# Performance work log

Hardware: AMD Instinct MI355X
Metric: run time of the kernel (lower is better)

Reference implementation:

```python
import jax, jax.numpy as jnp
import numpy as np
from jax import lax

HID = 1024
EXP = 2
INTER = HID * EXP          # 2048
STATE = 64
DT_RANK = INTER            # must equal INTER for the dt_bias broadcast in source
EPS = 1e-5


def _lin_w(k, i, o):
    return jax.random.normal(k, (i, o), jnp.float32) * (1.0 / np.sqrt(i))


def setup_inputs() -> dict:
    key = jax.random.key(0)
    ks = jax.random.split(key, 16)
    B, L = 4, 4096
    return {
        "x": jax.random.normal(ks[0], (B, L, HID), jnp.float32),
        "condition": jax.random.normal(ks[1], (B, HID), jnp.float32),
        "ln_g": jnp.ones((HID,), jnp.float32),
        "ln_b": jnp.zeros((HID,), jnp.float32),
        "W_in": _lin_w(ks[2], HID, 2 * INTER),
        "b_in": jnp.zeros((2 * INTER,), jnp.float32),
        "conv_w": jax.random.normal(ks[3], (INTER, 1, 3), jnp.float32) * 0.3,  # depthwise OIW
        "conv_b": jnp.zeros((INTER,), jnp.float32),
        "W_dt": _lin_w(ks[4], INTER, DT_RANK),
        "b_dt": jnp.zeros((DT_RANK,), jnp.float32),
        "dt_bias": jax.random.uniform(ks[5], (INTER,), jnp.float32),
        "A_log": jnp.log(jnp.arange(1, STATE + 1, dtype=jnp.float32)),
        "Dp": jnp.ones((INTER,), jnp.float32),
        "W_B": _lin_w(ks[6], INTER, STATE),
        "b_B": jnp.zeros((STATE,), jnp.float32),
        "W_C": _lin_w(ks[7], INTER, STATE),
        "b_C": jnp.zeros((STATE,), jnp.float32),
        "W_cond": _lin_w(ks[8], HID, INTER),
        "b_cond": jnp.zeros((INTER,), jnp.float32),
        "W_out": _lin_w(ks[9], INTER, HID),
        "b_out": jnp.zeros((HID,), jnp.float32),
    }


def _selective_scan(xp, W_dt, b_dt, dt_bias, A_log, Dp, W_B, b_B, W_C, b_C):
    B, L, Dm = xp.shape
    dt = jax.nn.softplus(xp @ W_dt + b_dt + dt_bias)          # [B,L,INTER]
    dt = jnp.mean(dt, axis=-1, keepdims=True)                  # [B,L,1]
    A = -jnp.exp(A_log)                                        # [STATE]
    A_disc = jnp.exp(A * dt)                                   # [B,L,STATE]
    Bx = (xp @ W_B + b_B) * dt * jnp.mean(xp, axis=-1, keepdims=True)  # B_disc * x_mean
    C = xp @ W_C + b_C                                         # [B,L,STATE]

    def step(h, inp):
        a, b, c = inp                                          # each [B,STATE]
        h = a * h + b
        return h, jnp.sum(c * h, axis=-1)                      # y_t: [B]

    h0 = jnp.zeros((B, STATE), xp.dtype)
    _, ys = lax.scan(step, h0, (A_disc.transpose(1, 0, 2),
                                Bx.transpose(1, 0, 2),
                                C.transpose(1, 0, 2)))         # ys: [L,B]
    y = ys.T[..., None]                                        # [B,L,1]
    return y + xp * Dp                                         # broadcast to [B,L,INTER]


def reference(x, condition, ln_g, ln_b, W_in, b_in, conv_w, conv_b, W_dt, b_dt,
              dt_bias, A_log, Dp, W_B, b_B, W_C, b_C, W_cond, b_cond, W_out, b_out):
    residual = x
    mu = jnp.mean(x, axis=-1, keepdims=True)
    var = jnp.mean((x - mu) ** 2, axis=-1, keepdims=True)
    xn = (x - mu) / jnp.sqrt(var + EPS) * ln_g + ln_b

    xproj2 = xn @ W_in + b_in                                  # [B,L,2*INTER]
    xproj, gate = jnp.split(xproj2, 2, axis=-1)

    # depthwise conv1d, kernel 3, padding 1
    xc = xproj.transpose(0, 2, 1)                              # [B,INTER,L]
    xc = lax.conv_general_dilated(xc, conv_w, (1,), [(1, 1)],
                                  dimension_numbers=("NCH", "OIH", "NCH"),
                                  feature_group_count=INTER)
    xc = xc + conv_b[None, :, None]
    xproj = xc.transpose(0, 2, 1)

    xproj = jax.nn.silu(xproj)
    xproj = xproj + (condition @ W_cond + b_cond)[:, None, :]

    y = _selective_scan(xproj, W_dt, b_dt, dt_bias, A_log, Dp, W_B, b_B, W_C, b_C)
    y = y * jax.nn.silu(gate)
    y = y @ W_out + b_out                                      # dropout is identity in eval
    return residual + y
```

## Files before the change

### kernel.cpp

```cpp
#include <hip/hip_runtime.h>
#include <stdint.h>

#define HID   1024
#define INTER 2048
#define NQK   4096
#define STATE 64
#define BSZ   4
#define LEN   4096
#define RTOT  (BSZ*LEN)
#define NCAT  2176
#define LC    128
#define NCH   (LEN/LC)

typedef unsigned short u16;
typedef u16   u16x4 __attribute__((ext_vector_type(4)));
typedef u16   u16x8 __attribute__((ext_vector_type(8)));
typedef float f32x4 __attribute__((ext_vector_type(4)));

__device__ __forceinline__ u16 f2bf(float f) {
  uint32_t u = __float_as_uint(f);
  u += 0x7fffu + ((u >> 16) & 1u);
  return (u16)(u >> 16);
}
__device__ __forceinline__ float bf2f(u16 h) {
  return __uint_as_float(((uint32_t)h) << 16);
}

typedef __attribute__((address_space(1))) void gvoid;
typedef __attribute__((address_space(3))) void lvoid;
__device__ __forceinline__ void gload16(const void* g, void* l) {
  __builtin_amdgcn_global_load_lds((gvoid*)(uintptr_t)g, (lvoid*)l, 16, 0, 0);
}

__device__ __forceinline__ void mfma16(f32x4 a, f32x4 b, f32x4& c) {
  asm volatile("v_mfma_f32_16x16x32_bf16 %0, %1, %2, %0" : "+v"(c) : "v"(a), "v"(b));
}

__global__ __launch_bounds__(256) void wconvT_kernel(const float* __restrict__ src,
                                                     u16* __restrict__ dst, int K, int N) {
  __shared__ float t[32][33];
  int tx = threadIdx.x & 31, ty = threadIdx.x >> 5;
  int n0 = blockIdx.x * 32, k0 = blockIdx.y * 32;
#pragma unroll
  for (int i = 0; i < 4; ++i)
    t[ty + 8*i][tx] = src[(size_t)(k0 + ty + 8*i) * N + n0 + tx];
  __syncthreads();
#pragma unroll
  for (int i = 0; i < 4; ++i)
    dst[(size_t)(n0 + ty + 8*i) * K + k0 + tx] = f2bf(t[tx][ty + 8*i]);
}

__global__ void bcat_kernel(const float* b_dt, const float* dt_bias, const float* b_B,
                            const float* b_C, float* bcat) {
  int i = blockIdx.x * 256 + threadIdx.x;
  if (i >= NCAT) return;
  float v;
  if (i < INTER) v = b_dt[i] + dt_bias[i];
  else if (i < INTER + STATE) v = b_B[i - INTER];
  else v = b_C[i - INTER - STATE];
  bcat[i] = v;
}

__global__ __launch_bounds__(256) void cond_kernel(const float* __restrict__ condition,
    const float* __restrict__ W, const float* __restrict__ bias, float* __restrict__ out) {
  int b = blockIdx.y;
  int j = blockIdx.x * 256 + threadIdx.x;
  float acc = bias[j];
  const float* crow = condition + b * HID;
  for (int k = 0; k < HID; ++k)
    acc = fmaf(crow[k], W[(size_t)k * INTER + j], acc);
  out[b * INTER + j] = acc;
}

__global__ __launch_bounds__(256) void ln_kernel(const float* __restrict__ x,
    const float* __restrict__ g, const float* __restrict__ bb, u16* __restrict__ xn) {
  int r = blockIdx.x;
  int tid = threadIdx.x;
  const float4 v = ((const float4*)(x + (size_t)r * HID))[tid];
  float s = v.x + v.y + v.z + v.w;
  float sq = v.x*v.x + v.y*v.y + v.z*v.z + v.w*v.w;
  for (int o = 32; o; o >>= 1) { s += __shfl_xor(s, o); sq += __shfl_xor(sq, o); }
  __shared__ float ps[4], pq[4];
  int wid = tid >> 6, lane = tid & 63;
  if (lane == 0) { ps[wid] = s; pq[wid] = sq; }
  __syncthreads();
  s = ps[0] + ps[1] + ps[2] + ps[3];
  sq = pq[0] + pq[1] + pq[2] + pq[3];
  float mu = s * (1.f / HID);
  float var = sq * (1.f / HID) - mu * mu;
  float rstd = rsqrtf(var + 1e-5f);
  int c = tid * 4;
  u16x4 ov;
  ov.x = f2bf((v.x - mu) * rstd * g[c+0] + bb[c+0]);
  ov.y = f2bf((v.y - mu) * rstd * g[c+1] + bb[c+1]);
  ov.z = f2bf((v.z - mu) * rstd * g[c+2] + bb[c+2]);
  ov.w = f2bf((v.w - mu) * rstd * g[c+3] + bb[c+3]);
  *(u16x4*)(xn + (size_t)r * HID + c) = ov;
}

template<int EPI>
__global__ __launch_bounds__(256) void gemm_bt(
    const u16* __restrict__ A, const u16* __restrict__ Bt, int K,
    const float* __restrict__ bias,
    u16* __restrict__ out0, u16* __restrict__ out1,
    float* __restrict__ dtsum, float* __restrict__ Bmat, float* __restrict__ Cmat,
    const float* __restrict__ resid, float* __restrict__ outf)
{
  __shared__ u16 lA[128 * 32];
  __shared__ u16 lB[128 * 32];
  const int tid = threadIdx.x;
  const int lane = tid & 63;
  const int wid = tid >> 6;
  const int wm = wid >> 1, wn = wid & 1;
  const int lr = lane & 15, lk = lane >> 4;
  const int col0 = blockIdx.x * 128;
  const int row0 = blockIdx.y * 128;
  const int wbase = tid & 192;

  f32x4 acc[4][4];
#pragma unroll
  for (int i = 0; i < 4; ++i)
#pragma unroll
    for (int j = 0; j < 4; ++j) acc[i][j] = (f32x4){0.f, 0.f, 0.f, 0.f};

  const size_t arow = (size_t)row0 * K;
  const size_t brow = (size_t)col0 * K;

  asm volatile("s_nop 7");
  for (int kt = 0; kt < K; kt += 32) {
    __syncthreads();
#pragma unroll
    for (int j = 0; j < 2; ++j) {
      int cbase = j * 256 + wbase;
      int chunk = cbase + lane;
      gload16(A + arow + (size_t)(chunk >> 2) * K + kt + (chunk & 3) * 8, &lA[cbase * 8]);
    }
#pragma unroll
    for (int j = 0; j < 2; ++j) {
      int cbase = j * 256 + wbase;
      int chunk = cbase + lane;
      gload16(Bt + brow + (size_t)(chunk >> 2) * K + kt + (chunk & 3) * 8, &lB[cbase * 8]);
    }
    __syncthreads();
    f32x4 aF[4], bF[4];
#pragma unroll
    for (int f = 0; f < 4; ++f)
      aF[f] = *(const f32x4*)&lA[(wm * 64 + f * 16 + lr) * 32 + lk * 8];
#pragma unroll
    for (int f = 0; f < 4; ++f)
      bF[f] = *(const f32x4*)&lB[(wn * 64 + f * 16 + lr) * 32 + lk * 8];
#pragma unroll
    for (int fm = 0; fm < 4; ++fm)
#pragma unroll
      for (int fn = 0; fn < 4; ++fn)
        mfma16(aF[fm], bF[fn], acc[fm][fn]);
  }
  asm volatile("s_nop 7\n\ts_nop 7\n\ts_nop 7");

  const int rb = row0 + wm * 64;
  const int cb = col0 + wn * 64;

  if constexpr (EPI == 0) {
#pragma unroll
    for (int fm = 0; fm < 4; ++fm)
#pragma unroll
      for (int fn = 0; fn < 4; ++fn)
#pragma unroll
        for (int rr = 0; rr < 4; ++rr) {
          int rowg = rb + fm * 16 + lk * 4 + rr;
          int colg = cb + fn * 16 + lr;
          float v = acc[fm][fn][rr] + bias[colg];
          if (colg < INTER) out0[(size_t)rowg * INTER + colg] = f2bf(v);
          else              out1[(size_t)rowg * INTER + colg - INTER] = f2bf(v);
        }
  } else if constexpr (EPI == 1) {
    if (col0 < INTER) {
#pragma unroll
      for (int fm = 0; fm < 4; ++fm)
#pragma unroll
        for (int rr = 0; rr < 4; ++rr) {
          float s = 0.f;
#pragma unroll
          for (int fn = 0; fn < 4; ++fn) {
            int colg = cb + fn * 16 + lr;
            float v = acc[fm][fn][rr] + bias[colg];
            s += (v > 20.f) ? v : log1pf(expf(v));
          }
#pragma unroll
          for (int o = 1; o < 16; o <<= 1) s += __shfl_xor(s, o);
          if (lr == 0) {
            int rowg = rb + fm * 16 + lk * 4 + rr;
            atomicAdd(&dtsum[rowg], s);
          }
        }
    } else {
#pragma unroll
      for (int fm = 0; fm < 4; ++fm)
#pragma unroll
        for (int fn = 0; fn < 4; ++fn)
#pragma unroll
          for (int rr = 0; rr < 4; ++rr) {
            int rowg = rb + fm * 16 + lk * 4 + rr;
            int colL = wn * 64 + fn * 16 + lr;
            float v = acc[fm][fn][rr] + bias[INTER + colL];
            if (colL < STATE) Bmat[(size_t)rowg * STATE + colL] = v;
            else              Cmat[(size_t)rowg * STATE + colL - STATE] = v;
          }
    }
  } else {
#pragma unroll
    for (int fm = 0; fm < 4; ++fm)
#pragma unroll
      for (int fn = 0; fn < 4; ++fn)
#pragma unroll
        for (int rr = 0; rr < 4; ++rr) {
          int rowg = rb + fm * 16 + lk * 4 + rr;
          int colg = cb + fn * 16 + lr;
          float v = acc[fm][fn][rr] + bias[colg];
          outf[(size_t)rowg * HID + colg] = v + resid[(size_t)rowg * HID + colg];
        }
  }
}

__global__ __launch_bounds__(256) void conv_kernel(
    const u16* __restrict__ xproj, const float* __restrict__ cw, const float* __restrict__ cbias,
    const float* __restrict__ condv, u16* __restrict__ xp, float* __restrict__ xpsum)
{
  int r = blockIdx.x;
  int b = r >> 12, l = r & (LEN - 1);
  int c0 = threadIdx.x * 8;
  const u16* base = xproj + (size_t)r * INTER + c0;
  u16x8 x0 = *(const u16x8*)base;
  u16x8 xm = (u16x8){0,0,0,0,0,0,0,0};
  u16x8 xpv = (u16x8){0,0,0,0,0,0,0,0};
  if (l > 0)       xm  = *(const u16x8*)(base - INTER);
  if (l < LEN - 1) xpv = *(const u16x8*)(base + INTER);
  float sum = 0.f;
  u16x8 ov;
#pragma unroll
  for (int j = 0; j < 8; ++j) {
    int c = c0 + j;
    float v = cw[c*3+0] * bf2f(xm[j]) + cw[c*3+1] * bf2f(x0[j]) + cw[c*3+2] * bf2f(xpv[j]) + cbias[c];
    float sg = v / (1.f + expf(-v));
    float o = sg + condv[b * INTER + c];
    sum += o;
    ov[j] = f2bf(o);
  }
  *(u16x8*)(xp + (size_t)r * INTER + c0) = ov;
  for (int o = 32; o; o >>= 1) sum += __shfl_xor(sum, o);
  __shared__ float ps[4];
  if ((threadIdx.x & 63) == 0) ps[threadIdx.x >> 6] = sum;
  __syncthreads();
  if (threadIdx.x == 0) xpsum[r] = ps[0] + ps[1] + ps[2] + ps[3];
}

__global__ __launch_bounds__(256) void scanprep_kernel(const float* __restrict__ A_log,
    const float* __restrict__ dtsum, const float* __restrict__ xpsum,
    const float* BmatIn, float* Adisc, float* Bx)
{
  int e = blockIdx.x * 256 + threadIdx.x;
  int r = e >> 6, s = e & 63;
  float dtm = dtsum[r] * (1.f / INTER);
  float xpm = xpsum[r] * (1.f / INTER);
  Adisc[e] = expf(-expf(A_log[s]) * dtm);
  Bx[e] = BmatIn[e] * dtm * xpm;
}

__global__ __launch_bounds__(64) void scanA_kernel(const float* __restrict__ Adisc,
    const float* __restrict__ Bx, float* __restrict__ cA, float* __restrict__ cB)
{
  int g = blockIdx.x; int b = g / NCH, ch = g % NCH;
  int s = threadIdx.x;
  float ap = 1.f, bacc = 0.f;
  size_t base = ((size_t)(b * LEN + ch * LC) << 6) + s;
  for (int i = 0; i < LC; ++i) {
    float a = Adisc[base], bb = Bx[base];
    bacc = fmaf(a, bacc, bb);
    ap *= a;
    base += 64;
  }
  cA[(size_t)g * 64 + s] = ap;
  cB[(size_t)g * 64 + s] = bacc;
}

__global__ __launch_bounds__(256) void scanB_kernel(const float* __restrict__ cA,
    const float* __restrict__ cB, float* __restrict__ hin)
{
  int t = threadIdx.x; int b = t >> 6, s = t & 63;
  float h = 0.f;
  for (int ch = 0; ch < NCH; ++ch) {
    size_t i = (size_t)(b * NCH + ch) * 64 + s;
    hin[i] = h;
    h = fmaf(cA[i], h, cB[i]);
  }
}

__global__ __launch_bounds__(64) void scanC_kernel(const float* __restrict__ Adisc,
    const float* __restrict__ Bx, const float* __restrict__ Cmat,
    const float* __restrict__ hin, float* __restrict__ yvec)
{
  int g = blockIdx.x; int b = g / NCH, ch = g % NCH;
  int s = threadIdx.x;
  float h = hin[(size_t)g * 64 + s];
  int l0 = ch * LC;
  size_t base = ((size_t)(b * LEN + l0) << 6) + s;
  for (int i = 0; i < LC; ++i) {
    h = fmaf(Adisc[base], h, Bx[base]);
    float p = Cmat[base] * h;
    for (int o = 32; o; o >>= 1) p += __shfl_xor(p, o);
    if (s == 0) yvec[b * LEN + l0 + i] = p;
    base += 64;
  }
}

__global__ __launch_bounds__(256) void yin_kernel(const u16* __restrict__ xp,
    const u16* __restrict__ gate, const float* __restrict__ yvec,
    const float* __restrict__ Dp, u16* __restrict__ yin)
{
  int i = blockIdx.x * 256 + threadIdx.x;
  int r = i >> 8;
  int c0 = (i & 255) * 8;
  size_t off = (size_t)r * INTER + c0;
  u16x8 xv = *(const u16x8*)(xp + off);
  u16x8 gv = *(const u16x8*)(gate + off);
  float yv = yvec[r];
  u16x8 ov;
#pragma unroll
  for (int j = 0; j < 8; ++j) {
    float g = bf2f(gv[j]);
    float sg = g / (1.f + expf(-g));
    float val = (yv + bf2f(xv[j]) * Dp[c0 + j]) * sg;
    ov[j] = f2bf(val);
  }
  *(u16x8*)(yin + off) = ov;
}

extern "C" void kernel_launch(void* const* d_in, const int* in_sizes, int n_in,
                              void* d_out, int out_size, void* d_ws, size_t ws_size,
                              hipStream_t stream) {
  (void)in_sizes; (void)n_in; (void)out_size; (void)ws_size;
  const float* x         = (const float*)d_in[0];
  const float* condition = (const float*)d_in[1];
  const float* ln_g      = (const float*)d_in[2];
  const float* ln_b      = (const float*)d_in[3];
  const float* W_in      = (const float*)d_in[4];
  const float* b_in      = (const float*)d_in[5];
  const float* conv_w    = (const float*)d_in[6];
  const float* conv_b    = (const float*)d_in[7];
  const float* W_dt      = (const float*)d_in[8];
  const float* b_dt      = (const float*)d_in[9];
  const float* dt_bias   = (const float*)d_in[10];
  const float* A_log     = (const float*)d_in[11];
  const float* Dp        = (const float*)d_in[12];
  const float* W_B       = (const float*)d_in[13];
  const float* b_B       = (const float*)d_in[14];
  const float* W_C       = (const float*)d_in[15];
  const float* b_C       = (const float*)d_in[16];
  const float* W_cond    = (const float*)d_in[17];
  const float* b_cond    = (const float*)d_in[18];
  const float* W_out     = (const float*)d_in[19];
  const float* b_out     = (const float*)d_in[20];

  char* ws = (char*)d_ws;
  u16*   wt_in  = (u16*)(ws + 0);
  u16*   wt_cat = (u16*)(ws + 8388608);
  u16*   wt_out = (u16*)(ws + 17301504);
  float* bcat   = (float*)(ws + 21495808);
  float* condv  = (float*)(ws + 21504512);
  float* dtsum  = (float*)(ws + 21537280);
  float* xpsum  = (float*)(ws + 21602816);
  float* yvec   = (float*)(ws + 21668352);
  float* cA     = (float*)(ws + 21733888);
  float* cB     = (float*)(ws + 21766656);
  float* hin    = (float*)(ws + 21799424);
  u16*   xn     = (u16*)(ws + 21832192);
  float* Bmat   = (float*)(ws + 21832192);
  float* Cmat   = (float*)(ws + 21832192 + 4194304);
  float* Adisc  = (float*)(ws + 21832192 + 8388608);
  u16*   xproj  = (u16*)(ws + 55386624);
  u16*   gate   = (u16*)(ws + 122495488);
  u16*   xp     = (u16*)(ws + 189604352);

  hipMemsetAsync(dtsum, 0, RTOT * 4, stream);

  wconvT_kernel<<<dim3(NQK/32, HID/32), 256, 0, stream>>>(W_in, wt_in, HID, NQK);
  wconvT_kernel<<<dim3(INTER/32, INTER/32), 256, 0, stream>>>(W_dt, wt_cat, INTER, INTER);
  wconvT_kernel<<<dim3(STATE/32, INTER/32), 256, 0, stream>>>(W_B, wt_cat + (size_t)2048*2048, INTER, STATE);
  wconvT_kernel<<<dim3(STATE/32, INTER/32), 256, 0, stream>>>(W_C, wt_cat + (size_t)2112*2048, INTER, STATE);
  wconvT_kernel<<<dim3(HID/32, INTER/32), 256, 0, stream>>>(W_out, wt_out, INTER, HID);
  bcat_kernel<<<dim3(9), 256, 0, stream>>>(b_dt, dt_bias, b_B, b_C, bcat);
  cond_kernel<<<dim3(INTER/256, BSZ), 256, 0, stream>>>(condition, W_cond, b_cond, condv);
  ln_kernel<<<dim3(RTOT), 256, 0, stream>>>(x, ln_g, ln_b, xn);

  gemm_bt<0><<<dim3(NQK/128, RTOT/128), 256, 0, stream>>>(
      xn, wt_in, HID, b_in, xproj, gate, nullptr, nullptr, nullptr, nullptr, nullptr);

  conv_kernel<<<dim3(RTOT), 256, 0, stream>>>(xproj, conv_w, conv_b, condv, xp, xpsum);

  gemm_bt<1><<<dim3(NCAT/128, RTOT/128), 256, 0, stream>>>(
      xp, wt_cat, INTER, bcat, nullptr, nullptr, dtsum, Bmat, Cmat, nullptr, nullptr);

  scanprep_kernel<<<dim3(RTOT*STATE/256), 256, 0, stream>>>(A_log, dtsum, xpsum, Bmat, Adisc, Bmat);
  scanA_kernel<<<dim3(BSZ*NCH), 64, 0, stream>>>(Adisc, Bmat, cA, cB);
  scanB_kernel<<<dim3(1), 256, 0, stream>>>(cA, cB, hin);
  scanC_kernel<<<dim3(BSZ*NCH), 64, 0, stream>>>(Adisc, Bmat, Cmat, hin, yvec);

  yin_kernel<<<dim3(RTOT*INTER/8/256), 256, 0, stream>>>(xp, gate, yvec, Dp, xproj);

  gemm_bt<2><<<dim3(HID/128, RTOT/128), 256, 0, stream>>>(
      xproj, wt_out, INTER, b_out, nullptr, nullptr, nullptr, nullptr, nullptr, x, (float*)d_out);
}
```

Before: 966.6 us.

## Replace 128x128 GEMMs with pipelined 256x256 tile kernel using swizzled LDS

Adds a new 512-thread GEMM kernel with 256x256 output tiles, K-step 64 split into halves, double-buffered direct-to-LDS loads issued between MFMA phases, an XOR-swizzled LDS layout, and a grouped block-index swizzle meant to improve L2 reuse. The three large GEMMs (input projection, dt projection, output projection) switch to it. The small B/C projection columns move into a separate launch of the old 128-tile kernel. The aim is to raise MFMA utilisation and cut LDS and global traffic per FLOP, at the cost of higher register/LDS use, hand-tuned waitcnt/barrier sequencing, and one extra kernel launch.

```diff
diff --git a/kernel.cpp b/kernel.cpp
--- a/kernel.cpp
+++ b/kernel.cpp
@@ -28,12 +28,20 @@
 
 typedef __attribute__((address_space(1))) void gvoid;
 typedef __attribute__((address_space(3))) void lvoid;
+typedef __attribute__((address_space(3))) u16 lds_u16;
 __device__ __forceinline__ void gload16(const void* g, void* l) {
   __builtin_amdgcn_global_load_lds((gvoid*)(uintptr_t)g, (lvoid*)l, 16, 0, 0);
 }
-
+__device__ __forceinline__ uint32_t lds_off(const u16* p) {
+  return (uint32_t)(uintptr_t)(lds_u16*)p;
+}
 __device__ __forceinline__ void mfma16(f32x4 a, f32x4 b, f32x4& c) {
   asm volatile("v_mfma_f32_16x16x32_bf16 %0, %1, %2, %0" : "+v"(c) : "v"(a), "v"(b));
+}
+__device__ __forceinline__ f32x4 dsread128(uint32_t off) {
+  f32x4 r;
+  asm volatile("ds_read_b128 %0, %1" : "=v"(r) : "v"(off));
+  return r;
 }
 
 __global__ __launch_bounds__(256) void wconvT_kernel(const float* __restrict__ src,
@@ -99,12 +107,163 @@
 }
 
 template<int EPI>
+__global__ __launch_bounds__(512, 2) void gemm256(
+    const u16* __restrict__ A, const u16* __restrict__ Bt, int K,
+    const float* __restrict__ bias,
+    u16* __restrict__ out0, u16* __restrict__ out1,
+    float* __restrict__ dtsum,
+    const float* __restrict__ resid, float* __restrict__ outf)
+{
+  __shared__ u16 sA[4 * 8192];
+  __shared__ u16 sB[4 * 8192];
+  const int tid = threadIdx.x;
+  const int lane = tid & 63, wid = tid >> 6;
+  const int wm = wid >> 2, wn = wid & 3;
+  const int lr = lane & 15, lk = lane >> 4;
+
+  const int nbx = gridDim.x;
+  const int nwg = nbx * gridDim.y;
+  const int flat = blockIdx.x + nbx * blockIdx.y;
+  const int cpx = nwg >> 3;
+  const int swz = (flat & 7) * cpx + (flat >> 3);
+  const int bx = swz % nbx, by = swz / nbx;
+  const int col0 = bx * 256, row0 = by * 256;
+  const int NT = K >> 6;
+
+  f32x4 acc[8][4];
+#pragma unroll
+  for (int i = 0; i < 8; ++i)
+#pragma unroll
+    for (int j = 0; j < 4; ++j) acc[i][j] = (f32x4){0.f, 0.f, 0.f, 0.f};
+
+  auto stA = [&](int kt, int kh, int bf) {
+#pragma unroll
+    for (int c = 0; c < 2; ++c) {
+      int rl = c * 128 + (tid >> 2);
+      int cl = (tid & 3) ^ (rl & 3);
+      const u16* src = A + (size_t)(row0 + rl) * K + kt * 64 + kh * 32 + cl * 8;
+      gload16(src, &sA[(bf * 2 + kh) * 8192 + c * 4096 + wid * 512]);
+    }
+  };
+  auto stB = [&](int kt, int kh, int bf) {
+#pragma unroll
+    for (int c = 0; c < 2; ++c) {
+      int rl = c * 128 + (tid >> 2);
+      int cl = (tid & 3) ^ (rl & 3);
+      const u16* src = Bt + (size_t)(col0 + rl) * K + kt * 64 + kh * 32 + cl * 8;
+      gload16(src, &sB[(bf * 2 + kh) * 8192 + c * 4096 + wid * 512]);
+    }
+  };
+
+  const uint32_t offA = lds_off(sA), offB = lds_off(sB);
+  const uint32_t chunkoff = (uint32_t)((lk ^ (lr & 3)) * 16);
+  const uint32_t rowA = (uint32_t)((wm * 128 + lr) * 64) + chunkoff;
+  const uint32_t rowB = (uint32_t)((wn * 64 + lr) * 64) + chunkoff;
+
+  stA(0, 0, 0); stB(0, 0, 0);
+  stA(0, 1, 0); stB(0, 1, 0);
+  stA(1, 0, 1); stB(1, 0, 1);
+  asm volatile("s_waitcnt vmcnt(8)" ::: "memory");
+  __builtin_amdgcn_s_barrier();
+  __builtin_amdgcn_sched_barrier(0);
+
+#define PHASE(J)                                                               \
+  {                                                                            \
+    const int kk = (J) >> 1, g = (J) & 1;                                      \
+    const uint32_t as = offA + (uint32_t)((p * 2 + kk) * 16384);               \
+    const uint32_t bs = offB + (uint32_t)((p * 2 + kk) * 16384);               \
+    f32x4 aF[4], bF[4];                                                        \
+    aF[0] = dsread128(as + rowA + (g * 4 + 0) * 1024);                         \
+    aF[1] = dsread128(as + rowA + (g * 4 + 1) * 1024);                         \
+    aF[2] = dsread128(as + rowA + (g * 4 + 2) * 1024);                         \
+    aF[3] = dsread128(as + rowA + (g * 4 + 3) * 1024);                         \
+    bF[0] = dsread128(bs + rowB + 0 * 1024);                                   \
+    bF[1] = dsread128(bs + rowB + 1 * 1024);                                   \
+    bF[2] = dsread128(bs + rowB + 2 * 1024);                                   \
+    bF[3] = dsread128(bs + rowB + 3 * 1024);                                   \
+    if ((J) == 0 && t + 1 < NT) stA(t + 1, 1, p ^ 1);                          \
+    if ((J) == 1 && t + 1 < NT) stB(t + 1, 1, p ^ 1);                          \
+    if ((J) == 2 && t + 2 < NT) stA(t + 2, 0, p);                              \
+    if ((J) == 3 && t + 2 < NT) stB(t + 2, 0, p);                              \
+    __builtin_amdgcn_s_barrier();                                              \
+    asm volatile("s_waitcnt lgkmcnt(0)" ::: "memory");                         \
+    __builtin_amdgcn_sched_barrier(0);                                         \
+    __builtin_amdgcn_s_setprio(1);                                             \
+    _Pragma("unroll")                                                          \
+    for (int f = 0; f < 4; ++f)                                                \
+      _Pragma("unroll")                                                        \
+      for (int n = 0; n < 4; ++n)                                              \
+        mfma16(aF[f], bF[n], acc[g * 4 + f][n]);                               \
+    __builtin_amdgcn_s_setprio(0);                                             \
+    if ((J) == 1 || (J) == 3)                                                  \
+      asm volatile("s_waitcnt vmcnt(6)" ::: "memory");                         \
+    __builtin_amdgcn_s_barrier();                                              \
+    __builtin_amdgcn_sched_barrier(0);                                         \
+  }
+
+  for (int t = 0; t < NT; ++t) {
+    const int p = t & 1;
+    PHASE(0)
+    PHASE(1)
+    PHASE(2)
+    PHASE(3)
+  }
+#undef PHASE
+
+  asm volatile("s_nop 7\n\ts_nop 7");
+
+  const int rb = row0 + wm * 128;
+  const int cb = col0 + wn * 64;
+
+  if constexpr (EPI == 0) {
+#pragma unroll
+    for (int fm = 0; fm < 8; ++fm)
+#pragma unroll
+      for (int fn = 0; fn < 4; ++fn)
+#pragma unroll
+        for (int rr = 0; rr < 4; ++rr) {
+          int rowg = rb + fm * 16 + lk * 4 + rr;
+          int colg = cb + fn * 16 + lr;
+          float v = acc[fm][fn][rr] + bias[colg];
+          if (col0 < INTER) out0[(size_t)rowg * INTER + colg] = f2bf(v);
+          else              out1[(size_t)rowg * INTER + colg - INTER] = f2bf(v);
+        }
+  } else if constexpr (EPI == 1) {
+#pragma unroll
+    for (int fm = 0; fm < 8; ++fm)
+#pragma unroll
+      for (int rr = 0; rr < 4; ++rr) {
+        float s = 0.f;
+#pragma unroll
+        for (int fn = 0; fn < 4; ++fn) {
+          int colg = cb + fn * 16 + lr;
+          float v = acc[fm][fn][rr] + bias[colg];
+          s += (v > 20.f) ? v : log1pf(expf(v));
+        }
+#pragma unroll
+        for (int o = 1; o < 16; o <<= 1) s += __shfl_xor(s, o);
+        if (lr == 0) atomicAdd(&dtsum[rb + fm * 16 + lk * 4 + rr], s);
+      }
+  } else {
+#pragma unroll
+    for (int fm = 0; fm < 8; ++fm)
+#pragma unroll
+      for (int fn = 0; fn < 4; ++fn)
+#pragma unroll
+        for (int rr = 0; rr < 4; ++rr) {
+          int rowg = rb + fm * 16 + lk * 4 + rr;
+          int colg = cb + fn * 16 + lr;
+          float v = acc[fm][fn][rr] + bias[colg];
+          outf[(size_t)rowg * HID + colg] = v + resid[(size_t)rowg * HID + colg];
+        }
+  }
+}
+
+template<int EPI>
 __global__ __launch_bounds__(256) void gemm_bt(
     const u16* __restrict__ A, const u16* __restrict__ Bt, int K,
     const float* __restrict__ bias,
-    u16* __restrict__ out0, u16* __restrict__ out1,
-    float* __restrict__ dtsum, float* __restrict__ Bmat, float* __restrict__ Cmat,
-    const float* __restrict__ resid, float* __restrict__ outf)
+    float* __restrict__ Bmat, float* __restrict__ Cmat)
 {
   __shared__ u16 lA[128 * 32];
   __shared__ u16 lB[128 * 32];
@@ -126,7 +285,6 @@
   const size_t arow = (size_t)row0 * K;
   const size_t brow = (size_t)col0 * K;
 
-  asm volatile("s_nop 7");
   for (int kt = 0; kt < K; kt += 32) {
     __syncthreads();
 #pragma unroll
@@ -155,12 +313,10 @@
       for (int fn = 0; fn < 4; ++fn)
         mfma16(aF[fm], bF[fn], acc[fm][fn]);
   }
-  asm volatile("s_nop 7\n\ts_nop 7\n\ts_nop 7");
+  asm volatile("s_nop 7\n\ts_nop 7");
 
   const int rb = row0 + wm * 64;
-  const int cb = col0 + wn * 64;
-
-  if constexpr (EPI == 0) {
+  if constexpr (EPI == 3) {
 #pragma unroll
     for (int fm = 0; fm < 4; ++fm)
 #pragma unroll
@@ -168,56 +324,10 @@
 #pragma unroll
         for (int rr = 0; rr < 4; ++rr) {
           int rowg = rb + fm * 16 + lk * 4 + rr;
-          int colg = cb + fn * 16 + lr;
-          float v = acc[fm][fn][rr] + bias[colg];
-          if (colg < INTER) out0[(size_t)rowg * INTER + colg] = f2bf(v);
-          else              out1[(size_t)rowg * INTER + colg - INTER] = f2bf(v);
-        }
-  } else if constexpr (EPI == 1) {
-    if (col0 < INTER) {
-#pragma unroll
-      for (int fm = 0; fm < 4; ++fm)
-#pragma unroll
-        for (int rr = 0; rr < 4; ++rr) {
-          float s = 0.f;
-#pragma unroll
-          for (int fn = 0; fn < 4; ++fn) {
-            int colg = cb + fn * 16 + lr;
-            float v = acc[fm][fn][rr] + bias[colg];
-            s += (v > 20.f) ? v : log1pf(expf(v));
-          }
-#pragma unroll
-          for (int o = 1; o < 16; o <<= 1) s += __shfl_xor(s, o);
-          if (lr == 0) {
-            int rowg = rb + fm * 16 + lk * 4 + rr;
-            atomicAdd(&dtsum[rowg], s);
-          }
-        }
-    } else {
-#pragma unroll
-      for (int fm = 0; fm < 4; ++fm)
-#pragma unroll
-        for (int fn = 0; fn < 4; ++fn)
-#pragma unroll
-          for (int rr = 0; rr < 4; ++rr) {
-            int rowg = rb + fm * 16 + lk * 4 + rr;
-            int colL = wn * 64 + fn * 16 + lr;
-            float v = acc[fm][fn][rr] + bias[INTER + colL];
-            if (colL < STATE) Bmat[(size_t)rowg * STATE + colL] = v;
-            else              Cmat[(size_t)rowg * STATE + colL - STATE] = v;
-          }
-    }
-  } else {
-#pragma unroll
-    for (int fm = 0; fm < 4; ++fm)
-#pragma unroll
-      for (int fn = 0; fn < 4; ++fn)
-#pragma unroll
-        for (int rr = 0; rr < 4; ++rr) {
-          int rowg = rb + fm * 16 + lk * 4 + rr;
-          int colg = cb + fn * 16 + lr;
-          float v = acc[fm][fn][rr] + bias[colg];
-          outf[(size_t)rowg * HID + colg] = v + resid[(size_t)rowg * HID + colg];
+          int colL = wn * 64 + fn * 16 + lr;
+          float v = acc[fm][fn][rr] + bias[colL];
+          if (colL < STATE) Bmat[(size_t)rowg * STATE + colL] = v;
+          else              Cmat[(size_t)rowg * STATE + colL - STATE] = v;
         }
   }
 }
@@ -392,13 +502,15 @@
   cond_kernel<<<dim3(INTER/256, BSZ), 256, 0, stream>>>(condition, W_cond, b_cond, condv);
   ln_kernel<<<dim3(RTOT), 256, 0, stream>>>(x, ln_g, ln_b, xn);
 
-  gemm_bt<0><<<dim3(NQK/128, RTOT/128), 256, 0, stream>>>(
-      xn, wt_in, HID, b_in, xproj, gate, nullptr, nullptr, nullptr, nullptr, nullptr);
+  gemm256<0><<<dim3(NQK/256, RTOT/256), 512, 0, stream>>>(
+      xn, wt_in, HID, b_in, xproj, gate, nullptr, nullptr, nullptr);
 
   conv_kernel<<<dim3(RTOT), 256, 0, stream>>>(xproj, conv_w, conv_b, condv, xp, xpsum);
 
-  gemm_bt<1><<<dim3(NCAT/128, RTOT/128), 256, 0, stream>>>(
-      xp, wt_cat, INTER, bcat, nullptr, nullptr, dtsum, Bmat, Cmat, nullptr, nullptr);
+  gemm256<1><<<dim3(INTER/256, RTOT/256), 512, 0, stream>>>(
+      xp, wt_cat, INTER, bcat, nullptr, nullptr, dtsum, nullptr, nullptr);
+  gemm_bt<3><<<dim3(1, RTOT/128), 256, 0, stream>>>(
+      xp, wt_cat + (size_t)2048*2048, INTER, bcat + INTER, Bmat, Cmat);
 
   scanprep_kernel<<<dim3(RTOT*STATE/256), 256, 0, stream>>>(A_log, dtsum, xpsum, Bmat, Adisc, Bmat);
   scanA_kernel<<<dim3(BSZ*NCH), 64, 0, stream>>>(Adisc, Bmat, cA, cB);
@@ -407,6 +519,6 @@
 
   yin_kernel<<<dim3(RTOT*INTER/8/256), 256, 0, stream>>>(xp, gate, yvec, Dp, xproj);
 
-  gemm_bt<2><<<dim3(HID/128, RTOT/128), 256, 0, stream>>>(
-      xproj, wt_out, INTER, b_out, nullptr, nullptr, nullptr, nullptr, nullptr, x, (float*)d_out);
-}
+  gemm256<2><<<dim3(HID/256, RTOT/256), 512, 0, stream>>>(
+      xproj, wt_out, INTER, b_out, nullptr, nullptr, nullptr, x, (float*)d_out);
+}
```

Result: no change. 965.0 us (-0.2%).
